# Kernel tuning notes

Measured on AMD Instinct MI355X. Metric: run time of the kernel, lower is better.

## Reference

```python
import jax, jax.numpy as jnp
import numpy as np

N_EMBD = 1024
N_HEAD = 16
B, L = 4, 2048


def setup_inputs() -> dict:
    key = jax.random.key(0)
    ks = jax.random.split(key, 5)
    scale = 1.0 / np.sqrt(N_EMBD)
    x = jax.random.normal(ks[0], (B, L, N_EMBD), dtype=jnp.float32)
    # nn.Linear(n_embd, n_embd, bias=False) weights, stored torch-style (out, in)
    Wq = jax.random.uniform(ks[1], (N_EMBD, N_EMBD), jnp.float32, -scale, scale)
    Wk = jax.random.uniform(ks[2], (N_EMBD, N_EMBD), jnp.float32, -scale, scale)
    Wv = jax.random.uniform(ks[3], (N_EMBD, N_EMBD), jnp.float32, -scale, scale)
    Wp = jax.random.uniform(ks[4], (N_EMBD, N_EMBD), jnp.float32, -scale, scale)
    attn_mask = jnp.ones((B, L), dtype=jnp.int32)
    return {"x": x, "Wq": Wq, "Wk": Wk, "Wv": Wv, "Wp": Wp, "attn_mask": attn_mask}


def reference(x, Wq, Wk, Wv, Wp, attn_mask):
    Bq, Lq, C = x.shape
    hd = C // N_HEAD
    # torch Linear: y = x @ W.T
    def split_heads(y):
        return y.reshape(Bq, Lq, N_HEAD, hd).transpose(0, 2, 1, 3)  # (B,H,L,hd)
    q = split_heads(x @ Wq.T)
    k = split_heads(x @ Wk.T)
    v = split_heads(x @ Wv.T)
    att = jnp.einsum("bhqd,bhkd->bhqk", q, k) / np.sqrt(hd)  # (B,H,L,L)
    causal = jnp.tril(jnp.ones((Lq, Lq), dtype=bool))
    neg_inf = jnp.float32(-jnp.inf)
    att = jnp.where(causal[None, None, :, :], att, neg_inf)
    pad = (attn_mask != 0)[:, None, None, :]  # (B,1,1,L) key-side padding mask
    att = jnp.where(pad, att, neg_inf)
    att = jax.nn.softmax(att, axis=-1)
    y = jnp.einsum("bhqk,bhkd->bhqd", att, v)
    y = y.transpose(0, 2, 1, 3).reshape(Bq, Lq, C)
    return y @ Wp.T
```

## Files before the change

kernel.cpp:

```cpp
#include <hip/hip_runtime.h>

typedef __attribute__((ext_vector_type(8))) short short8;
typedef __attribute__((ext_vector_type(4))) float floatx4;

#define CEMB 1024
#define NHEAD 16
#define HD 64
#define BATCH 4
#define SEQ 2048

#define BARRIER() asm volatile("s_waitcnt lgkmcnt(0)\n\ts_barrier" ::: "memory")

__device__ __forceinline__ unsigned short f2bf(float f) {
    union { float f; unsigned int i; } x; x.f = f;
    unsigned int r = x.i + 0x7FFFu + ((x.i >> 16) & 1u);
    return (unsigned short)(r >> 16);
}
__device__ __forceinline__ unsigned int packbf_trunc(float a, float b) {
    union { float f; unsigned int u; } x, y; x.f = a; y.f = b;
    return (x.u >> 16) | (y.u & 0xFFFF0000u);
}

#define GLD16(gp, lp) \
    __builtin_amdgcn_global_load_lds((const __attribute__((address_space(1))) void*)(gp), \
                                     (__attribute__((address_space(3))) void*)(lp), 16, 0, 0)

__global__ void cast_x(const float* __restrict__ src, unsigned short* __restrict__ dst, int n4) {
    int i = blockIdx.x * blockDim.x + threadIdx.x;
    if (i < n4) {
        float4 v = ((const float4*)src)[i];
        ushort4 o;
        o.x = f2bf(v.x); o.y = f2bf(v.y); o.z = f2bf(v.z); o.w = f2bf(v.w);
        ((ushort4*)dst)[i] = o;
    }
}

__global__ void cast_w(const float* __restrict__ w0, const float* __restrict__ w1,
                       const float* __restrict__ w2, const float* __restrict__ w3,
                       unsigned short* __restrict__ o0, unsigned short* __restrict__ o1,
                       unsigned short* __restrict__ o2, unsigned short* __restrict__ o3) {
    int which = blockIdx.y;
    const float* src = which == 0 ? w0 : which == 1 ? w1 : which == 2 ? w2 : w3;
    unsigned short* dst = which == 0 ? o0 : which == 1 ? o1 : which == 2 ? o2 : o3;
    float scale = (which == 0) ? 0.125f : 1.0f;
    int i = blockIdx.x * blockDim.x + threadIdx.x;
    float4 v = ((const float4*)src)[i];
    ushort4 o;
    o.x = f2bf(v.x * scale); o.y = f2bf(v.y * scale);
    o.z = f2bf(v.z * scale); o.w = f2bf(v.w * scale);
    ((ushort4*)dst)[i] = o;
}

__launch_bounds__(256)
__global__ void gemm128(const unsigned short* __restrict__ A,
                        const unsigned short* __restrict__ W0,
                        const unsigned short* __restrict__ W1,
                        const unsigned short* __restrict__ W2,
                        void* __restrict__ O0, void* __restrict__ O1, void* __restrict__ O2,
                        int mode) {
    const unsigned short* W = (blockIdx.z == 0) ? W0 : (blockIdx.z == 1 ? W1 : W2);
    void* outp = (blockIdx.z == 0) ? O0 : (blockIdx.z == 1 ? O1 : O2);

    __shared__ unsigned short As[128 * 32];
    __shared__ unsigned short Bs[128 * 32];

    int tid = threadIdx.x;
    int wave = tid >> 6;
    int lane = tid & 63;
    int l16 = lane & 15;
    int quad = lane >> 4;
    int wm = wave >> 1, wn = wave & 1;
    int m0 = blockIdx.y * 128;
    int n0 = blockIdx.x * 128;

    int rl = lane >> 2;
    int cpos = lane & 3;
    int clog = cpos ^ ((rl >> 1) & 3);
    int seg = wave * 2;
    const unsigned short* aSrc0 = A + (size_t)(m0 + seg * 16 + rl) * CEMB + clog * 8;
    const unsigned short* aSrc1 = aSrc0 + 16 * CEMB;
    const unsigned short* bSrc0 = W + (size_t)(n0 + seg * 16 + rl) * CEMB + clog * 8;
    const unsigned short* bSrc1 = bSrc0 + 16 * CEMB;
    unsigned short* aDst0 = As + seg * 16 * 32;
    unsigned short* aDst1 = aDst0 + 16 * 32;
    unsigned short* bDst0 = Bs + seg * 16 * 32;
    unsigned short* bDst1 = bDst0 + 16 * 32;

    int rchunk = quad ^ ((l16 >> 1) & 3);
    const unsigned short* aRd = As + (wm * 64 + l16) * 32 + rchunk * 8;
    const unsigned short* bRd = Bs + (wn * 64 + l16) * 32 + rchunk * 8;

    floatx4 acc[4][4];
    #pragma unroll
    for (int t = 0; t < 4; ++t)
        #pragma unroll
        for (int u = 0; u < 4; ++u) acc[t][u] = (floatx4){0.f, 0.f, 0.f, 0.f};

    for (int k0 = 0; k0 < CEMB; k0 += 32) {
        GLD16(aSrc0 + k0, aDst0);
        GLD16(aSrc1 + k0, aDst1);
        GLD16(bSrc0 + k0, bDst0);
        GLD16(bSrc1 + k0, bDst1);
        __syncthreads();

        short8 aF[4], bF[4];
        #pragma unroll
        for (int t = 0; t < 4; ++t) aF[t] = *(const short8*)(aRd + t * 16 * 32);
        #pragma unroll
        for (int u = 0; u < 4; ++u) bF[u] = *(const short8*)(bRd + u * 16 * 32);
        #pragma unroll
        for (int t = 0; t < 4; ++t)
            #pragma unroll
            for (int u = 0; u < 4; ++u)
                acc[t][u] = __builtin_amdgcn_mfma_f32_16x16x32_bf16(aF[t], bF[u], acc[t][u], 0, 0, 0);
        __syncthreads();
    }

    if (mode == 1) {
        #pragma unroll
        for (int t = 0; t < 4; ++t)
            #pragma unroll
            for (int j = 0; j < 4; ++j) {
                int m = m0 + wm * 64 + t * 16 + quad * 4 + j;
                #pragma unroll
                for (int u = 0; u < 4; ++u) {
                    int n = n0 + wn * 64 + u * 16 + l16;
                    ((float*)outp)[(size_t)m * CEMB + n] = acc[t][u][j];
                }
            }
    } else if (blockIdx.z < 2) {
        #pragma unroll
        for (int t = 0; t < 4; ++t)
            #pragma unroll
            for (int j = 0; j < 4; ++j) {
                int m = m0 + wm * 64 + t * 16 + quad * 4 + j;
                int bb = m >> 11, ll = m & (SEQ - 1);
                #pragma unroll
                for (int u = 0; u < 4; ++u) {
                    int n = n0 + wn * 64 + u * 16 + l16;
                    int h = n >> 6, d = n & (HD - 1);
                    ((unsigned short*)outp)[(size_t)((bb * NHEAD + h) * SEQ + ll) * HD + d] =
                        f2bf(acc[t][u][j]);
                }
            }
    } else {
        #pragma unroll
        for (int t = 0; t < 4; ++t) {
            int m = m0 + wm * 64 + t * 16 + quad * 4;
            int bb = m >> 11, ll = m & (SEQ - 1);
            #pragma unroll
            for (int u = 0; u < 4; ++u) {
                int n = n0 + wn * 64 + u * 16 + l16;
                int h = n >> 6, d = n & (HD - 1);
                ushort4 o4;
                o4.x = f2bf(acc[t][u][0]); o4.y = f2bf(acc[t][u][1]);
                o4.z = f2bf(acc[t][u][2]); o4.w = f2bf(acc[t][u][3]);
                *(ushort4*)&((unsigned short*)outp)[(size_t)((bb * NHEAD + h) * HD + d) * SEQ + ll] = o4;
            }
        }
    }
}

__launch_bounds__(256, 2)
__global__ void attn_mfma(const unsigned short* __restrict__ Qb,
                          const unsigned short* __restrict__ Kb,
                          const unsigned short* __restrict__ Vtg,
                          const int* __restrict__ amask,
                          unsigned short* __restrict__ Yb) {
    __shared__ unsigned short Ks[64 * 64];
    __shared__ unsigned short Vs[64 * 64];
    __shared__ unsigned short Ps[128 * 64];

    int tid = threadIdx.x;
    int wave = tid >> 6;
    int lane = tid & 63;
    int l16 = lane & 15;
    int quad = lane >> 4;
    int l7 = l16 & 7;
    int pair = blockIdx.x;
    int bh = blockIdx.y;
    int bidx = bh >> 4;
    int h = bh & (NHEAD - 1);
    size_t hbase = (size_t)bh * SEQ * HD;

    int r0 = tid >> 3, p0 = tid & 7;
    int cl = p0 ^ (r0 & 7);
    unsigned short* kDst0 = Ks + r0 * 64 + p0 * 8;
    unsigned short* kDst1 = kDst0 + 32 * 64;
    unsigned short* vDst0 = Vs + r0 * 64 + p0 * 8;
    unsigned short* vDst1 = vDst0 + 32 * 64;
    const unsigned short* kSrc0 = Kb + hbase + (size_t)r0 * HD + cl * 8;
    const unsigned short* kSrc1 = kSrc0 + (size_t)32 * HD;
    const unsigned short* vSrc0 = Vtg + hbase + (size_t)r0 * SEQ + cl * 8;
    const unsigned short* vSrc1 = vSrc0 + (size_t)32 * SEQ;
    const int* mSrc = amask + bidx * SEQ + quad * 4;

    #pragma unroll
    for (int pass = 0; pass < 2; ++pass) {
        int qt = pass == 0 ? (15 - pair) : pair;
        int q0 = qt * 128;
        int nkt = 2 * qt + 2;

        short8 qf[2][2];
        #pragma unroll
        for (int qsub = 0; qsub < 2; ++qsub)
            #pragma unroll
            for (int kk = 0; kk < 2; ++kk)
                qf[qsub][kk] = *(const short8*)(Qb + hbase +
                    (size_t)(q0 + wave * 32 + qsub * 16 + l16) * HD + kk * 32 + quad * 8);

        short8 kr0 = *(const short8*)(kSrc0);
        short8 kr1 = *(const short8*)(kSrc1);
        short8 vr0 = *(const short8*)(vSrc0);
        short8 vr1 = *(const short8*)(vSrc1);
        int4 cmi[4];
        #pragma unroll
        for (int t = 0; t < 4; ++t) cmi[t] = *(const int4*)(mSrc + t * 16);

        floatx4 o[2][4];
        #pragma unroll
        for (int qsub = 0; qsub < 2; ++qsub)
            #pragma unroll
            for (int t = 0; t < 4; ++t) o[qsub][t] = (floatx4){0.f, 0.f, 0.f, 0.f};
        float ls[2] = {0.f, 0.f};

        int qw = q0 + wave * 32;

        for (int jt = 0; jt < nkt; ++jt) {
            BARRIER();
            *(short8*)kDst0 = kr0;
            *(short8*)kDst1 = kr1;
            *(short8*)vDst0 = vr0;
            *(short8*)vDst1 = vr1;
            int4 cm[4];
            #pragma unroll
            for (int t = 0; t < 4; ++t) cm[t] = cmi[t];
            if (jt + 1 < nkt) {
                size_t ko = (size_t)(jt + 1) * 64;
                kr0 = *(const short8*)(kSrc0 + ko * HD);
                kr1 = *(const short8*)(kSrc1 + ko * HD);
                vr0 = *(const short8*)(vSrc0 + ko);
                vr1 = *(const short8*)(vSrc1 + ko);
                #pragma unroll
                for (int t = 0; t < 4; ++t) cmi[t] = *(const int4*)(mSrc + (jt + 1) * 64 + t * 16);
            }
            BARRIER();

            if (jt * 64 <= qw + 31) {
                floatx4 sc[2][4];
                #pragma unroll
                for (int qsub = 0; qsub < 2; ++qsub)
                    #pragma unroll
                    for (int t = 0; t < 4; ++t) sc[qsub][t] = (floatx4){0.f, 0.f, 0.f, 0.f};
                #pragma unroll
                for (int kk = 0; kk < 2; ++kk)
                    #pragma unroll
                    for (int t = 0; t < 4; ++t) {
                        short8 aK = *(const short8*)(Ks + (t * 16 + l16) * 64 +
                                                     ((kk * 4 + quad) ^ l7) * 8);
                        #pragma unroll
                        for (int qsub = 0; qsub < 2; ++qsub)
                            sc[qsub][t] = __builtin_amdgcn_mfma_f32_16x16x32_bf16(
                                aK, qf[qsub][kk], sc[qsub][t], 0, 0, 0);
                    }

                bool needc = (jt * 64 + 63 > qw);

                #pragma unroll
                for (int qsub = 0; qsub < 2; ++qsub) {
                    int qi = q0 + wave * 32 + qsub * 16 + l16;
                    #pragma unroll
                    for (int t = 0; t < 4; ++t) {
                        int kb = jt * 64 + t * 16 + quad * 4;
                        float p[4];
                        #pragma unroll
                        for (int j = 0; j < 4; ++j) {
                            float sv = sc[qsub][t][j];
                            if (needc) sv = (kb + j <= qi) ? sv : -1e30f;
                            sv = cm[t][j] ? sv : -1e30f;
                            p[j] = __expf(sv);
                            ls[qsub] += p[j];
                        }
                        int row = wave * 32 + qsub * 16 + l16;
                        int pos = (t * 2 + (quad >> 1)) ^ l7;
                        uint2 pk;
                        pk.x = packbf_trunc(p[0], p[1]);
                        pk.y = packbf_trunc(p[2], p[3]);
                        *(uint2*)(Ps + row * 64 + pos * 8 + (quad & 1) * 4) = pk;
                    }
                }

                #pragma unroll
                for (int kk = 0; kk < 2; ++kk) {
                    short8 pa[2];
                    #pragma unroll
                    for (int qsub = 0; qsub < 2; ++qsub)
                        pa[qsub] = *(const short8*)(Ps + (wave * 32 + qsub * 16 + l16) * 64 +
                                                    ((kk * 4 + quad) ^ l7) * 8);
                    #pragma unroll
                    for (int t = 0; t < 4; ++t) {
                        short8 vb = *(const short8*)(Vs + (t * 16 + l16) * 64 +
                                                     ((kk * 4 + quad) ^ l7) * 8);
                        #pragma unroll
                        for (int qsub = 0; qsub < 2; ++qsub)
                            o[qsub][t] = __builtin_amdgcn_mfma_f32_16x16x32_bf16(
                                pa[qsub], vb, o[qsub][t], 0, 0, 0);
                    }
                }
            }
        }

        #pragma unroll
        for (int qsub = 0; qsub < 2; ++qsub) {
            ls[qsub] += __shfl_xor(ls[qsub], 16, 64);
            ls[qsub] += __shfl_xor(ls[qsub], 32, 64);
        }

        #pragma unroll
        for (int qsub = 0; qsub < 2; ++qsub)
            #pragma unroll
            for (int j = 0; j < 4; ++j) {
                float lq = __shfl(ls[qsub], quad * 4 + j, 64);
                float inv = 1.0f / lq;
                size_t row = (size_t)bidx * SEQ + q0 + wave * 32 + qsub * 16 + quad * 4 + j;
                #pragma unroll
                for (int t = 0; t < 4; ++t)
                    Yb[row * CEMB + h * HD + t * 16 + l16] = f2bf(o[qsub][t][j] * inv);
            }
    }
}

extern "C" void kernel_launch(void* const* d_in, const int* in_sizes, int n_in,
                              void* d_out, int out_size, void* d_ws, size_t ws_size,
                              hipStream_t stream) {
    const float* x  = (const float*)d_in[0];
    const float* Wq = (const float*)d_in[1];
    const float* Wk = (const float*)d_in[2];
    const float* Wv = (const float*)d_in[3];
    const float* Wp = (const float*)d_in[4];
    const int* amask = (const int*)d_in[5];

    char* ws = (char*)d_ws;
    unsigned short* xb  = (unsigned short*)(ws + 0);
    unsigned short* Wqb = (unsigned short*)(ws + (16u << 20));
    unsigned short* Wkb = (unsigned short*)(ws + (18u << 20));
    unsigned short* Wvb = (unsigned short*)(ws + (20u << 20));
    unsigned short* Wpb = (unsigned short*)(ws + (22u << 20));
    unsigned short* Qb  = (unsigned short*)(ws + (24u << 20));
    unsigned short* Kb  = (unsigned short*)(ws + (40u << 20));
    unsigned short* Vtg = (unsigned short*)(ws + (56u << 20));
    unsigned short* Yb  = (unsigned short*)(ws + (72u << 20));

    const int NX4 = (BATCH * SEQ * CEMB) / 4;
    const int NW4 = (CEMB * CEMB) / 4;
    cast_x<<<dim3(NX4 / 256), 256, 0, stream>>>(x, xb, NX4);
    cast_w<<<dim3(NW4 / 256, 4), 256, 0, stream>>>(Wq, Wk, Wv, Wp, Wqb, Wkb, Wvb, Wpb);

    gemm128<<<dim3(CEMB / 128, (BATCH * SEQ) / 128, 3), 256, 0, stream>>>(
        xb, Wqb, Wkb, Wvb, (void*)Qb, (void*)Kb, (void*)Vtg, 0);

    attn_mfma<<<dim3(8, BATCH * NHEAD), 256, 0, stream>>>(Qb, Kb, Vtg, amask, Yb);

    gemm128<<<dim3(CEMB / 128, (BATCH * SEQ) / 128, 1), 256, 0, stream>>>(
        Yb, Wpb, nullptr, nullptr, d_out, nullptr, nullptr, 1);
}
```

Before: 286.7 us.

## Replace 128x128 GEMM with double-buffered 256x256 tile GEMM and XCD-aware remap

```diff
diff --git a/kernel.cpp b/kernel.cpp
--- a/kernel.cpp
+++ b/kernel.cpp
@@ -51,111 +51,173 @@
     ((ushort4*)dst)[i] = o;
 }
 
-__launch_bounds__(256)
-__global__ void gemm128(const unsigned short* __restrict__ A,
-                        const unsigned short* __restrict__ W0,
-                        const unsigned short* __restrict__ W1,
-                        const unsigned short* __restrict__ W2,
-                        void* __restrict__ O0, void* __restrict__ O1, void* __restrict__ O2,
-                        int mode) {
-    const unsigned short* W = (blockIdx.z == 0) ? W0 : (blockIdx.z == 1 ? W1 : W2);
-    void* outp = (blockIdx.z == 0) ? O0 : (blockIdx.z == 1 ? O1 : O2);
-
-    __shared__ unsigned short As[128 * 32];
-    __shared__ unsigned short Bs[128 * 32];
+
+#define PHASE(Ab, Bb, mh, nh) do {                                              \
+    short8 af[4][2], bfr[2][2];                                                 \
+    _Pragma("unroll")                                                           \
+    for (int mm = 0; mm < 4; ++mm) {                                            \
+        af[mm][0] = *(const short8*)((Ab) + aOffR + (mh)*4096 + mm*1024 + ck0); \
+        af[mm][1] = *(const short8*)((Ab) + aOffR + (mh)*4096 + mm*1024 + ck1); \
+    }                                                                           \
+    _Pragma("unroll")                                                           \
+    for (int nn = 0; nn < 2; ++nn) {                                            \
+        bfr[nn][0] = *(const short8*)((Bb) + bOffR + (nh)*2048 + nn*1024 + ck0);\
+        bfr[nn][1] = *(const short8*)((Bb) + bOffR + (nh)*2048 + nn*1024 + ck1);\
+    }                                                                           \
+    __builtin_amdgcn_s_setprio(1);                                              \
+    _Pragma("unroll")                                                           \
+    for (int mm = 0; mm < 4; ++mm)                                              \
+        _Pragma("unroll")                                                       \
+        for (int nn = 0; nn < 2; ++nn) {                                        \
+            acc[(mh)*4+mm][(nh)*2+nn] = __builtin_amdgcn_mfma_f32_16x16x32_bf16(\
+                af[mm][0], bfr[nn][0], acc[(mh)*4+mm][(nh)*2+nn], 0, 0, 0);     \
+            acc[(mh)*4+mm][(nh)*2+nn] = __builtin_amdgcn_mfma_f32_16x16x32_bf16(\
+                af[mm][1], bfr[nn][1], acc[(mh)*4+mm][(nh)*2+nn], 0, 0, 0);     \
+        }                                                                       \
+    __builtin_amdgcn_s_setprio(0);                                              \
+    __builtin_amdgcn_sched_barrier(0);                                          \
+} while (0)
+
+#define STAGE(Ab, Bb, k0) do {                                                  \
+    GLD16(aS + (k0),              (Ab) + aL);                                   \
+    GLD16(aS + (k0) +  8 * CEMB,  (Ab) + aL + 512);                             \
+    GLD16(aS + (k0) + 16 * CEMB,  (Ab) + aL + 1024);                            \
+    GLD16(aS + (k0) + 24 * CEMB,  (Ab) + aL + 1536);                            \
+    GLD16(bS + (k0),              (Bb) + aL);                                   \
+    GLD16(bS + (k0) +  8 * CEMB,  (Bb) + aL + 512);                             \
+    GLD16(bS + (k0) + 16 * CEMB,  (Bb) + aL + 1024);                            \
+    GLD16(bS + (k0) + 24 * CEMB,  (Bb) + aL + 1536);                            \
+} while (0)
+
+#define PHASE4(Ab, Bb, t, do_stage) do {                                        \
+    short8 af[4][2], bfr[2][2];                                                 \
+    _Pragma("unroll")                                                           \
+    for (int mm = 0; mm < 4; ++mm) {                                            \
+        af[mm][0] = *(const short8*)((Ab) + aOffR + 4096 + mm*1024 + ck0);      \
+        af[mm][1] = *(const short8*)((Ab) + aOffR + 4096 + mm*1024 + ck1);      \
+    }                                                                           \
+    _Pragma("unroll")                                                           \
+    for (int nn = 0; nn < 2; ++nn) {                                            \
+        bfr[nn][0] = *(const short8*)((Bb) + bOffR + 2048 + nn*1024 + ck0);     \
+        bfr[nn][1] = *(const short8*)((Bb) + bOffR + 2048 + nn*1024 + ck1);     \
+    }                                                                           \
+    asm volatile("s_waitcnt lgkmcnt(0)\n\ts_barrier" ::: "memory");             \
+    __builtin_amdgcn_sched_barrier(0);                                          \
+    if (do_stage) STAGE(Ab, Bb, ((t) + 2) * 64);                                \
+    __builtin_amdgcn_s_setprio(1);                                              \
+    _Pragma("unroll")                                                           \
+    for (int mm = 0; mm < 4; ++mm)                                              \
+        _Pragma("unroll")                                                       \
+        for (int nn = 0; nn < 2; ++nn) {                                        \
+            acc[4+mm][2+nn] = __builtin_amdgcn_mfma_f32_16x16x32_bf16(          \
+                af[mm][0], bfr[nn][0], acc[4+mm][2+nn], 0, 0, 0);               \
+            acc[4+mm][2+nn] = __builtin_amdgcn_mfma_f32_16x16x32_bf16(          \
+                af[mm][1], bfr[nn][1], acc[4+mm][2+nn], 0, 0, 0);               \
+        }                                                                       \
+    __builtin_amdgcn_s_setprio(0);                                              \
+    __builtin_amdgcn_sched_barrier(0);                                          \
+} while (0)
+
+#define TILE(t, VMN, do_stage) do {                                             \
+    unsigned short* Ab = &As[(t) & 1][0];                                       \
+    unsigned short* Bb = &Bs[(t) & 1][0];                                       \
+    asm volatile("s_waitcnt vmcnt(" #VMN ")\n\ts_barrier" ::: "memory");        \
+    PHASE(Ab, Bb, 0, 0);                                                        \
+    PHASE(Ab, Bb, 1, 0);                                                        \
+    PHASE(Ab, Bb, 0, 1);                                                        \
+    PHASE4(Ab, Bb, t, do_stage);                                                \
+} while (0)
+
+__launch_bounds__(512, 2)
+__global__ void gemm256(const unsigned short* __restrict__ A,
+                        const unsigned short* __restrict__ W,
+                        void* __restrict__ O0, void* __restrict__ O1,
+                        void* __restrict__ O2, int mode, int ntn) {
+    __shared__ unsigned short As[2][16384];
+    __shared__ unsigned short Bs[2][16384];
+
+    int nwg = gridDim.x;
+    int bid = blockIdx.x;
+    int wg = (bid & 7) * (nwg >> 3) + (bid >> 3);
+    int mt = wg / ntn;
+    int nt = wg - mt * ntn;
+    int m0 = mt * 256, n0 = nt * 256;
 
     int tid = threadIdx.x;
-    int wave = tid >> 6;
-    int lane = tid & 63;
-    int l16 = lane & 15;
-    int quad = lane >> 4;
-    int wm = wave >> 1, wn = wave & 1;
-    int m0 = blockIdx.y * 128;
-    int n0 = blockIdx.x * 128;
-
-    int rl = lane >> 2;
-    int cpos = lane & 3;
-    int clog = cpos ^ ((rl >> 1) & 3);
-    int seg = wave * 2;
-    const unsigned short* aSrc0 = A + (size_t)(m0 + seg * 16 + rl) * CEMB + clog * 8;
-    const unsigned short* aSrc1 = aSrc0 + 16 * CEMB;
-    const unsigned short* bSrc0 = W + (size_t)(n0 + seg * 16 + rl) * CEMB + clog * 8;
-    const unsigned short* bSrc1 = bSrc0 + 16 * CEMB;
-    unsigned short* aDst0 = As + seg * 16 * 32;
-    unsigned short* aDst1 = aDst0 + 16 * 32;
-    unsigned short* bDst0 = Bs + seg * 16 * 32;
-    unsigned short* bDst1 = bDst0 + 16 * 32;
-
-    int rchunk = quad ^ ((l16 >> 1) & 3);
-    const unsigned short* aRd = As + (wm * 64 + l16) * 32 + rchunk * 8;
-    const unsigned short* bRd = Bs + (wn * 64 + l16) * 32 + rchunk * 8;
-
-    floatx4 acc[4][4];
+    int wave = tid >> 6, lane = tid & 63;
+    int l16 = lane & 15, quad = lane >> 4;
+    int wm = wave >> 2, wn = wave & 3;
+
+    int srow = lane >> 3;
+    int scol = ((lane & 7) ^ srow) * 8;
+    const unsigned short* aS = A + (size_t)(m0 + wave * 32 + srow) * CEMB + scol;
+    const unsigned short* bS = W + (size_t)(n0 + wave * 32 + srow) * CEMB + scol;
+    int aL = wave * 2048;
+
+    int aOffR = (wm * 128 + l16) * 64;
+    int bOffR = (wn * 64 + l16) * 64;
+    int ck0 = (quad ^ (l16 & 7)) * 8;
+    int ck1 = ck0 ^ 32;
+
+    floatx4 acc[8][4];
     #pragma unroll
-    for (int t = 0; t < 4; ++t)
-        #pragma unroll
-        for (int u = 0; u < 4; ++u) acc[t][u] = (floatx4){0.f, 0.f, 0.f, 0.f};
-
-    for (int k0 = 0; k0 < CEMB; k0 += 32) {
-        GLD16(aSrc0 + k0, aDst0);
-        GLD16(aSrc1 + k0, aDst1);
-        GLD16(bSrc0 + k0, bDst0);
-        GLD16(bSrc1 + k0, bDst1);
-        __syncthreads();
-
-        short8 aF[4], bF[4];
-        #pragma unroll
-        for (int t = 0; t < 4; ++t) aF[t] = *(const short8*)(aRd + t * 16 * 32);
-        #pragma unroll
-        for (int u = 0; u < 4; ++u) bF[u] = *(const short8*)(bRd + u * 16 * 32);
-        #pragma unroll
-        for (int t = 0; t < 4; ++t)
-            #pragma unroll
-            for (int u = 0; u < 4; ++u)
-                acc[t][u] = __builtin_amdgcn_mfma_f32_16x16x32_bf16(aF[t], bF[u], acc[t][u], 0, 0, 0);
-        __syncthreads();
-    }
+    for (int mm = 0; mm < 8; ++mm)
+        #pragma unroll
+        for (int nn = 0; nn < 4; ++nn) acc[mm][nn] = (floatx4){0.f, 0.f, 0.f, 0.f};
+
+    STAGE(&As[0][0], &Bs[0][0], 0);
+    STAGE(&As[1][0], &Bs[1][0], 64);
+
+    #pragma unroll 2
+    for (int t = 0; t < 14; ++t) { TILE(t, 8, true); }
+    TILE(14, 8, false);
+    TILE(15, 0, false);
 
     if (mode == 1) {
-        #pragma unroll
-        for (int t = 0; t < 4; ++t)
+        float* Of = (float*)O0;
+        #pragma unroll
+        for (int mf = 0; mf < 8; ++mf)
             #pragma unroll
             for (int j = 0; j < 4; ++j) {
-                int m = m0 + wm * 64 + t * 16 + quad * 4 + j;
-                #pragma unroll
-                for (int u = 0; u < 4; ++u) {
-                    int n = n0 + wn * 64 + u * 16 + l16;
-                    ((float*)outp)[(size_t)m * CEMB + n] = acc[t][u][j];
-                }
-            }
-    } else if (blockIdx.z < 2) {
-        #pragma unroll
-        for (int t = 0; t < 4; ++t)
-            #pragma unroll
-            for (int j = 0; j < 4; ++j) {
-                int m = m0 + wm * 64 + t * 16 + quad * 4 + j;
-                int bb = m >> 11, ll = m & (SEQ - 1);
-                #pragma unroll
-                for (int u = 0; u < 4; ++u) {
-                    int n = n0 + wn * 64 + u * 16 + l16;
-                    int h = n >> 6, d = n & (HD - 1);
-                    ((unsigned short*)outp)[(size_t)((bb * NHEAD + h) * SEQ + ll) * HD + d] =
-                        f2bf(acc[t][u][j]);
+                int m = m0 + wm * 128 + mf * 16 + quad * 4 + j;
+                #pragma unroll
+                for (int nf = 0; nf < 4; ++nf) {
+                    int n = n0 + wn * 64 + nf * 16 + l16;
+                    Of[(size_t)m * CEMB + n] = acc[mf][nf][j];
                 }
             }
     } else {
-        #pragma unroll
-        for (int t = 0; t < 4; ++t) {
-            int m = m0 + wm * 64 + t * 16 + quad * 4;
-            int bb = m >> 11, ll = m & (SEQ - 1);
-            #pragma unroll
-            for (int u = 0; u < 4; ++u) {
-                int n = n0 + wn * 64 + u * 16 + l16;
-                int h = n >> 6, d = n & (HD - 1);
-                ushort4 o4;
-                o4.x = f2bf(acc[t][u][0]); o4.y = f2bf(acc[t][u][1]);
-                o4.z = f2bf(acc[t][u][2]); o4.w = f2bf(acc[t][u][3]);
-                *(ushort4*)&((unsigned short*)outp)[(size_t)((bb * NHEAD + h) * HD + d) * SEQ + ll] = o4;
+        int which = n0 >> 10;
+        unsigned short* out = (unsigned short*)(which == 0 ? O0 : which == 1 ? O1 : O2);
+        if (which < 2) {
+            #pragma unroll
+            for (int mf = 0; mf < 8; ++mf)
+                #pragma unroll
+                for (int j = 0; j < 4; ++j) {
+                    int m = m0 + wm * 128 + mf * 16 + quad * 4 + j;
+                    int bb = m >> 11, ll = m & (SEQ - 1);
+                    #pragma unroll
+                    for (int nf = 0; nf < 4; ++nf) {
+                        int n = (n0 & (CEMB - 1)) + wn * 64 + nf * 16 + l16;
+                        int h = n >> 6, d = n & (HD - 1);
+                        out[(size_t)((bb * NHEAD + h) * SEQ + ll) * HD + d] =
+                            f2bf(acc[mf][nf][j]);
+                    }
+                }
+        } else {
+            #pragma unroll
+            for (int mf = 0; mf < 8; ++mf) {
+                int m = m0 + wm * 128 + mf * 16 + quad * 4;
+                int bb = m >> 11, ll = m & (SEQ - 1);
+                #pragma unroll
+                for (int nf = 0; nf < 4; ++nf) {
+                    int n = (n0 & (CEMB - 1)) + wn * 64 + nf * 16 + l16;
+                    int h = n >> 6, d = n & (HD - 1);
+                    ushort4 o4;
+                    o4.x = f2bf(acc[mf][nf][0]); o4.y = f2bf(acc[mf][nf][1]);
+                    o4.z = f2bf(acc[mf][nf][2]); o4.w = f2bf(acc[mf][nf][3]);
+                    *(ushort4*)&out[(size_t)((bb * NHEAD + h) * HD + d) * SEQ + ll] = o4;
+                }
             }
         }
     }
@@ -356,11 +418,11 @@
     cast_x<<<dim3(NX4 / 256), 256, 0, stream>>>(x, xb, NX4);
     cast_w<<<dim3(NW4 / 256, 4), 256, 0, stream>>>(Wq, Wk, Wv, Wp, Wqb, Wkb, Wvb, Wpb);
 
-    gemm128<<<dim3(CEMB / 128, (BATCH * SEQ) / 128, 3), 256, 0, stream>>>(
-        xb, Wqb, Wkb, Wvb, (void*)Qb, (void*)Kb, (void*)Vtg, 0);
+    gemm256<<<dim3(32 * 12), 512, 0, stream>>>(
+        xb, Wqb, (void*)Qb, (void*)Kb, (void*)Vtg, 0, 12);
 
     attn_mfma<<<dim3(8, BATCH * NHEAD), 256, 0, stream>>>(Qb, Kb, Vtg, amask, Yb);
 
-    gemm128<<<dim3(CEMB / 128, (BATCH * SEQ) / 128, 1), 256, 0, stream>>>(
-        Yb, Wpb, nullptr, nullptr, d_out, nullptr, nullptr, 1);
-}
+    gemm256<<<dim3(32 * 4), 512, 0, stream>>>(
+        Yb, Wpb, d_out, nullptr, nullptr, 1, 4);
+}
```

Result: faster. 278.4 us (-2.9%).
